# Optimization experiments

Hardware: AMD Instinct MI355X
Metric: run time of the kernel (lower is better)

Reference implementation:

```python
import jax, jax.numpy as jnp
import numpy as np

N = 16384   # total nodes in batch
E = 65536   # edges
B = 512     # sessions
L = 32      # nodes per session
H = 64      # hidden_size
HEADS = 16  # GAT heads (layer 1)
K = 3       # interests
V = 32000   # n_node (item vocab)
NEG = 0.2   # leaky relu slope


def _u(k, shape, stdv):
    return jax.random.uniform(k, shape, jnp.float32, -stdv, stdv)


def setup_inputs():
    key = jax.random.key(0)
    ks = jax.random.split(key, 24)
    s = 1.0 / np.sqrt(H)  # reset_parameters: uniform(-stdv, stdv)
    D = K * H
    return {
        "x": jax.random.randint(ks[0], (N,), 0, V),
        "edge_index": jax.random.randint(ks[1], (2, E), 0, N),
        "batch": jnp.repeat(jnp.arange(B, dtype=jnp.int32), L),
        "embedding": _u(ks[2], (V, H), s),
        "w_interest": _u(ks[3], (H, K), s),
        "gat1_W": _u(ks[4], (K, H, HEADS * H), s),
        "gat1_as": _u(ks[5], (K, HEADS, H), s),
        "gat1_ad": _u(ks[6], (K, HEADS, H), s),
        "gat1_b": _u(ks[7], (K, HEADS * H), s),
        "gat2_W": _u(ks[8], (K, HEADS * H, H), s),
        "gat2_as": _u(ks[9], (K, 1, H), s),
        "gat2_ad": _u(ks[10], (K, 1, H), s),
        "gat2_b": _u(ks[11], (K, H), s),
        "W1_w": _u(ks[12], (D, D), s), "W1_b": _u(ks[13], (D,), s),
        "W2_w": _u(ks[14], (D, D), s), "W2_b": _u(ks[15], (D,), s),
        "q_w": _u(ks[16], (D, 1), s), "q_b": _u(ks[17], (1,), s),
        "W3_w": _u(ks[18], (2 * D, D), s), "W3_b": _u(ks[19], (D,), s),
    }


def _gat(h_in, W, b, a_s, a_d, src, dst, valid, heads, out):
    """PyG GATConv: per-head linear, edge softmax over dest, self-loops for all nodes."""
    n = h_in.shape[0]
    h = (h_in @ W).reshape(n, heads, out)          # [n, heads, out]
    asrc = (h * a_s[None]).sum(-1)                 # [n, heads]
    adst = (h * a_d[None]).sum(-1)
    loop = jnp.arange(n)
    fs = jnp.concatenate([src, loop])              # edges + self-loops
    fd = jnp.concatenate([dst, loop])
    v = jnp.concatenate([valid, jnp.ones((n,), bool)])
    logits = jax.nn.leaky_relu(asrc[fs] + adst[fd], NEG)   # [E+n, heads]
    logits = jnp.where(v[:, None], logits, -1e9)
    m = jax.ops.segment_max(logits, fd, num_segments=n)
    p = jnp.exp(logits - m[fd]) * v[:, None]
    denom = jax.ops.segment_sum(p, fd, num_segments=n)     # [n, heads]
    num = jax.ops.segment_sum(p[:, :, None] * h[fs], fd, num_segments=n)
    return (num / denom[:, :, None]).reshape(n, heads * out) + b


def _model(x, edge_index, batch, embedding, w_interest,
           gat1_W, gat1_as, gat1_ad, gat1_b,
           gat2_W, gat2_as, gat2_ad, gat2_b,
           W1_w, W1_b, W2_w, W2_b, q_w, q_b, W3_w, W3_b):
    e = embedding[x]                                # [N, H]
    g = jax.nn.softmax((e @ w_interest) / 0.1, axis=-1)   # [N, K]
    mask = g > (1.0 / K)                            # interest_mask
    src, dst = edge_index[0], edge_index[1]
    hiddens = []
    for i in range(K):                              # fixed small interest loop
        xi = g[:, i:i + 1] * e                      # einsum('ik,il->ikl')[:, i]
        valid = mask[src, i] & mask[dst, i]         # subgraph edge mask
        h1 = jax.nn.relu(_gat(xi, gat1_W[i], gat1_b[i], gat1_as[i], gat1_ad[i],
                              src, dst, valid, HEADS, H))
        h2 = _gat(h1, gat2_W[i], gat2_b[i], gat2_as[i], gat2_ad[i],
                  src, dst, valid, 1, H)
        hiddens.append(h2)
    sess = jnp.concatenate(hiddens, axis=1)         # [N, K*H]
    # Embedding2Score
    last_idx = jax.ops.segment_max(jnp.arange(N), batch, num_segments=B)
    v_n = sess[last_idx]                            # [B, K*H]  last node per session
    q1 = v_n[batch] @ W1_w + W1_b                   # v_n repeated per node
    q2 = sess @ W2_w + W2_b
    alpha = jax.nn.sigmoid(q1 + q2) @ q_w + q_b     # [N, 1]
    s_g = jax.ops.segment_sum(alpha * sess, batch, num_segments=B)
    s_h = jnp.concatenate([v_n, s_g], axis=1) @ W3_w + W3_b   # [B, K*H]
    s_h = s_h.reshape(B * K, H)                     # multi-interest split
    z = s_h @ embedding.T                           # [B*K, V]
    return z.reshape(B, K, V).max(axis=1)           # [B, V]


def reference(x, edge_index, batch, embedding, w_interest,
              gat1_W, gat1_as, gat1_ad, gat1_b,
              gat2_W, gat2_as, gat2_ad, gat2_b,
              W1_w, W1_b, W2_w, W2_b, q_w, q_b, W3_w, W3_b):
    return _model(x, edge_index, batch, embedding, w_interest,
                  gat1_W, gat1_as, gat1_ad, gat1_b,
                  gat2_W, gat2_as, gat2_ad, gat2_b,
                  W1_w, W1_b, W2_w, W2_b, q_w, q_b, W3_w, W3_b)
```

## Files before the change

kernel.cpp:

```cpp
#include <hip/hip_runtime.h>
#include <math.h>

#define NN 16384
#define EE 65536
#define BB 512
#define VV 32000

typedef unsigned short us_t;
typedef unsigned int u32_t;
typedef __attribute__((ext_vector_type(4))) float f32x4;
typedef __attribute__((ext_vector_type(8))) short bf16x8;

__device__ __forceinline__ float bf2f(unsigned int u) {
  return __uint_as_float((u & 0xffffu) << 16);
}
__device__ __forceinline__ unsigned short f2bf(float f) {
  unsigned int x = __float_as_uint(f);
  unsigned int r = (x + 0x7fffu + ((x >> 16) & 1u)) >> 16;
  return (unsigned short)r;
}
__device__ __forceinline__ float wsum(float v) {
#pragma unroll
  for (int o = 32; o; o >>= 1) v += __shfl_xor(v, o, 64);
  return v;
}
__device__ __forceinline__ float redu16(float v) {
  v += __shfl_xor(v, 1, 64);
  v += __shfl_xor(v, 2, 64);
  v += __shfl_xor(v, 4, 64);
  v += __shfl_xor(v, 8, 64);
  return v;
}
__device__ __forceinline__ float lrelu(float x) { return x > 0.f ? x : 0.2f * x; }

__global__ void k_detect(const void* emb, int* flag) {
  if (threadIdx.x == 0 && blockIdx.x == 0) {
    const us_t* u = (const us_t*)emb;
    int ok = 1;
    for (int i = 0; i < 128; i++) {
      float v = bf2f((unsigned int)u[i]);
      if (!(fabsf(v) <= 0.13f)) { ok = 0; break; }
    }
    *flag = ok;
  }
}

struct PrepArgs {
  const void* src[17];
  void* dst[17];
  int n[17];
  int kind[17];
  int start[18];
};

__global__ void k_prep(PrepArgs pa, const int* __restrict__ flag) {
  int blk = blockIdx.x;
  int s = 0;
  while (s < 16 && blk >= pa.start[s + 1]) s++;
  int i = (blk - pa.start[s]) * 256 + threadIdx.x;
  if (i >= pa.n[s]) return;
  float v = (*flag) ? bf2f((unsigned int)((const us_t*)pa.src[s])[i])
                    : ((const float*)pa.src[s])[i];
  int kind = pa.kind[s];
  if (kind == 0) {
    ((float*)pa.dst[s])[i] = v;
  } else if (kind == 1) {
    ((us_t*)pa.dst[s])[i] = f2bf(v);
  } else if (kind == 2) {
    int ii = i >> 16, r = i & 65535, k = r >> 10, col = r & 1023;
    ((us_t*)pa.dst[s])[(ii << 16) + col * 64 + k] = f2bf(v);
  } else if (kind == 3) {
    int ii = i >> 16, r = i & 65535, k = r >> 6, col = r & 63;
    ((us_t*)pa.dst[s])[(ii << 16) + col * 1024 + k] = f2bf(v);
  } else {
    int k = i / 192, col = i % 192;
    ((us_t*)pa.dst[s])[col * 192 + k] = f2bf(v);
  }
}

__global__ void k_prepWa(const void* __restrict__ g1Wraw,
                         const float* __restrict__ g1as, const float* __restrict__ g1ad,
                         const int* __restrict__ flag, us_t* __restrict__ Waspack) {
  int gid = blockIdx.x * 256 + threadIdx.x;
  if (gid >= 96 * 64) return;
  int c = gid >> 6, k = gid & 63;
  int i = c >> 5, sd = (c >> 4) & 1, h = c & 15;
  const float* av = (sd ? g1ad : g1as) + i * 1024 + h * 64;
  size_t base = (size_t)i * 65536 + (size_t)k * 1024 + h * 64;
  int isbf = *flag;
  float s = 0.f;
  for (int d = 0; d < 64; d++) {
    float wv = isbf ? bf2f((unsigned int)((const us_t*)g1Wraw)[base + d])
                    : ((const float*)g1Wraw)[base + d];
    s += wv * av[d];
  }
  Waspack[c * 64 + k] = f2bf(s);
}

__global__ void k_embed(const int* __restrict__ x, const void* __restrict__ embr,
                        const void* __restrict__ wintr, const int* __restrict__ flag,
                        us_t* __restrict__ e_bf, float* __restrict__ g) {
  int gid = blockIdx.x * blockDim.x + threadIdx.x;
  int n = gid >> 6, lane = gid & 63;
  if (n >= NN) return;
  int isbf = *flag;
  size_t ei = (size_t)x[n] * 64 + lane;
  float v = isbf ? bf2f((unsigned int)((const us_t*)embr)[ei]) : ((const float*)embr)[ei];
  e_bf[(size_t)n * 64 + lane] = f2bf(v);
  float w0, w1, w2;
  if (isbf) {
    const us_t* w = (const us_t*)wintr;
    w0 = bf2f(w[lane * 3 + 0]); w1 = bf2f(w[lane * 3 + 1]); w2 = bf2f(w[lane * 3 + 2]);
  } else {
    const float* w = (const float*)wintr;
    w0 = w[lane * 3 + 0]; w1 = w[lane * 3 + 1]; w2 = w[lane * 3 + 2];
  }
  float t0 = wsum(v * w0), t1 = wsum(v * w1), t2 = wsum(v * w2);
  if (lane == 0) {
    float l0 = t0 / 0.1f, l1 = t1 / 0.1f, l2 = t2 / 0.1f;
    float m = fmaxf(l0, fmaxf(l1, l2));
    float p0 = __expf(l0 - m), p1 = __expf(l1 - m), p2 = __expf(l2 - m);
    float inv = 1.0f / (p0 + p1 + p2);
    g[n * 4 + 0] = p0 * inv; g[n * 4 + 1] = p1 * inv;
    g[n * 4 + 2] = p2 * inv; g[n * 4 + 3] = 0.f;
  }
}

__global__ void k_countv(const int* __restrict__ ei, const float* __restrict__ g,
                         int* __restrict__ countsv) {
  int e = blockIdx.x * 256 + threadIdx.x;
  if (e >= EE) return;
  int s = ei[e], d = ei[EE + e];
  const float thr = 1.0f / 3.0f;
#pragma unroll
  for (int i = 0; i < 3; i++) {
    if (g[s * 4 + i] > thr && g[d * 4 + i] > thr)
      atomicAdd(&countsv[i * NN + d], 1);
  }
}

__global__ void k_scanv(const int* __restrict__ counts, int* __restrict__ offsets) {
  __shared__ int part[256];
  __shared__ int excl[257];
  int t = threadIdx.x;
  int base = t * 192;
  int s = 0;
  for (int j = 0; j < 192; j++) s += counts[base + j];
  part[t] = s;
  __syncthreads();
  if (t == 0) {
    int run = 0;
    for (int j = 0; j < 256; j++) { excl[j] = run; run += part[j]; }
    excl[256] = run;
  }
  __syncthreads();
  int run = excl[t];
  for (int j = 0; j < 192; j++) { offsets[base + j] = run; run += counts[base + j]; }
  if (t == 255) offsets[3 * NN] = excl[256];
}

__global__ void k_fillv(const int* __restrict__ ei, const float* __restrict__ g,
                        const float* __restrict__ eatt,
                        const int* __restrict__ offsetsv, int* __restrict__ fillposv,
                        int2* __restrict__ edgesC, float* __restrict__ easrcP) {
  int e = blockIdx.x * 256 + threadIdx.x;
  if (e >= EE) return;
  int s = ei[e], d = ei[EE + e];
  const float thr = 1.0f / 3.0f;
#pragma unroll
  for (int i = 0; i < 3; i++) {
    float gs = g[s * 4 + i];
    if (gs > thr && g[d * 4 + i] > thr) {
      int pos = offsetsv[i * NN + d] + atomicAdd(&fillposv[i * NN + d], 1);
      edgesC[pos] = make_int2(s, __float_as_int(gs));
      const float* er = &eatt[(size_t)s * 96 + i * 32];
      float* op = &easrcP[(size_t)pos * 16];
#pragma unroll
      for (int h = 0; h < 16; h++) op[h] = gs * er[h];
    }
  }
}

__global__ __launch_bounds__(256) void k_easrc(
    const us_t* __restrict__ e_bf, const us_t* __restrict__ Waspack,
    float* __restrict__ eatt) {
  __shared__ char As[8192];
  int t = threadIdx.x;
  int row0 = blockIdx.x * 64;
  for (int id = t; id < 512; id += 256) {
    int r = id >> 3, c = id & 7;
    uint4 v = *(const uint4*)&e_bf[(size_t)(row0 + r) * 64 + c * 8];
    *(uint4*)(As + r * 128 + ((c ^ (r & 7)) << 4)) = v;
  }
  __syncthreads();
  int wv = t >> 6, L = t & 63, li = L & 15, lq = L >> 4;
#pragma unroll
  for (int ct = 0; ct < 6; ct++) {
    f32x4 acc = {0.f, 0.f, 0.f, 0.f};
#pragma unroll
    for (int ks = 0; ks < 2; ks++) {
      int row = wv * 16 + li;
      bf16x8 af = *(const bf16x8*)(As + row * 128 + (((ks * 4 + lq) ^ (row & 7)) << 4));
      bf16x8 bfr = *(const bf16x8*)(Waspack + (size_t)(ct * 16 + li) * 64 + ks * 32 + lq * 8);
      acc = __builtin_amdgcn_mfma_f32_16x16x32_bf16(af, bfr, acc, 0, 0, 0);
    }
#pragma unroll
    for (int r = 0; r < 4; r++) {
      int row = row0 + wv * 16 + lq * 4 + r;
      eatt[(size_t)row * 96 + ct * 16 + li] = acc[r];
    }
  }
}

__global__ __launch_bounds__(256) void k_gat_fused(
    const us_t* __restrict__ e_bf, const float* __restrict__ g,
    const float* __restrict__ eatt, const us_t* __restrict__ g1Wt,
    const us_t* __restrict__ g2Wt, const float* __restrict__ b1all,
    const float* __restrict__ g2as, const float* __restrict__ g2ad,
    const int* __restrict__ offsetsv, const int2* __restrict__ edgesC,
    const float* __restrict__ easrcP,
    float* __restrict__ h2pre, float* __restrict__ a2s, float* __restrict__ a2d) {
  __shared__ char xagg[32 * 2048];
  __shared__ char Tbuf[2][32 * 128];
  __shared__ float a2sl[32], a2dl[32];
  int t = threadIdx.x;
  int intr = blockIdx.y;
  int n0 = blockIdx.x * 32;
  int wv = t >> 6, L = t & 63, li = L & 15, lq = L >> 4;
  const us_t* Wt1 = g1Wt + (size_t)intr * 65536;
  const us_t* Wt2 = g2Wt + (size_t)intr * 65536;
  const float* b1 = b1all + intr * 1024;
  const float* as2 = g2as + intr * 64;
  const float* ad2 = g2ad + intr * 64;
  if (t < 32) { a2sl[t] = 0.f; a2dl[t] = 0.f; }
  int h = L >> 2;
  int doff = (L & 3) * 16;
  for (int k = 0; k < 8; k++) {
    int nl = wv * 8 + k;
    int n = n0 + nl;
    float gn = g[n * 4 + intr];
    float ad = gn * eatt[(size_t)n * 96 + intr * 32 + 16 + h];
    float m = lrelu(gn * eatt[(size_t)n * 96 + intr * 32 + h] + ad);
    float den = 1.f;
    float acc[16];
    {
      const uint4* ep = (const uint4*)&e_bf[(size_t)n * 64 + doff];
      uint4 a = ep[0], b = ep[1];
      acc[0] = gn * bf2f(a.x);  acc[1] = gn * bf2f(a.x >> 16);
      acc[2] = gn * bf2f(a.y);  acc[3] = gn * bf2f(a.y >> 16);
      acc[4] = gn * bf2f(a.z);  acc[5] = gn * bf2f(a.z >> 16);
      acc[6] = gn * bf2f(a.w);  acc[7] = gn * bf2f(a.w >> 16);
      acc[8] = gn * bf2f(b.x);  acc[9] = gn * bf2f(b.x >> 16);
      acc[10] = gn * bf2f(b.y); acc[11] = gn * bf2f(b.y >> 16);
      acc[12] = gn * bf2f(b.z); acc[13] = gn * bf2f(b.z >> 16);
      acc[14] = gn * bf2f(b.w); acc[15] = gn * bf2f(b.w >> 16);
    }
    int beg = offsetsv[intr * NN + n], end = offsetsv[intr * NN + n + 1];
    for (int j = beg; j < end; j++) {
      int2 sg = edgesC[j];
      int s = sg.x;
      float gs = __int_as_float(sg.y);
      float l = lrelu(easrcP[(size_t)j * 16 + h] + ad);
      float p = __expf(l - m);
      den += p;
      float pg = p * gs;
      const uint4* ep = (const uint4*)&e_bf[(size_t)s * 64 + doff];
      uint4 a = ep[0], b = ep[1];
      acc[0] += pg * bf2f(a.x);  acc[1] += pg * bf2f(a.x >> 16);
      acc[2] += pg * bf2f(a.y);  acc[3] += pg * bf2f(a.y >> 16);
      acc[4] += pg * bf2f(a.z);  acc[5] += pg * bf2f(a.z >> 16);
      acc[6] += pg * bf2f(a.w);  acc[7] += pg * bf2f(a.w >> 16);
      acc[8] += pg * bf2f(b.x);  acc[9] += pg * bf2f(b.x >> 16);
      acc[10] += pg * bf2f(b.y); acc[11] += pg * bf2f(b.y >> 16);
      acc[12] += pg * bf2f(b.z); acc[13] += pg * bf2f(b.z >> 16);
      acc[14] += pg * bf2f(b.w); acc[15] += pg * bf2f(b.w >> 16);
    }
    float inv = 1.f / den;
    u32_t w[8];
#pragma unroll
    for (int kk = 0; kk < 8; kk++) {
      w[kk] = (u32_t)f2bf(acc[2 * kk] * inv) | ((u32_t)f2bf(acc[2 * kk + 1] * inv) << 16);
    }
    int c0 = h * 8 + (L & 3) * 2;
    *(uint4*)(xagg + nl * 2048 + ((c0 ^ (nl & 7)) << 4)) = make_uint4(w[0], w[1], w[2], w[3]);
    *(uint4*)(xagg + nl * 2048 + (((c0 + 1) ^ (nl & 7)) << 4)) = make_uint4(w[4], w[5], w[6], w[7]);
  }
  __syncthreads();
  int rt = wv & 1, ctb = (wv >> 1) * 2;
  f32x4 acc2[2];
  acc2[0] = {0.f, 0.f, 0.f, 0.f};
  acc2[1] = {0.f, 0.f, 0.f, 0.f};
  for (int hh = 0; hh < 16; hh++) {
    f32x4 c1[2];
    c1[0] = {0.f, 0.f, 0.f, 0.f};
    c1[1] = {0.f, 0.f, 0.f, 0.f};
#pragma unroll
    for (int ks = 0; ks < 2; ks++) {
      int row = rt * 16 + li;
      int ca = hh * 8 + ks * 4 + lq;
      bf16x8 af = *(const bf16x8*)(xagg + row * 2048 + ((ca ^ (row & 7)) << 4));
#pragma unroll
      for (int c2 = 0; c2 < 2; c2++) {
        int oc = hh * 64 + (ctb + c2) * 16 + li;
        bf16x8 bfr = *(const bf16x8*)(Wt1 + (size_t)oc * 64 + ks * 32 + lq * 8);
        c1[c2] = __builtin_amdgcn_mfma_f32_16x16x32_bf16(af, bfr, c1[c2], 0, 0, 0);
      }
    }
    char* Tb = Tbuf[hh & 1];
#pragma unroll
    for (int c2 = 0; c2 < 2; c2++) {
      int col = (ctb + c2) * 16 + li;
      float bv = b1[hh * 64 + col];
#pragma unroll
      for (int r = 0; r < 4; r++) {
        int row = rt * 16 + lq * 4 + r;
        float tv = fmaxf(c1[c2][r] + bv, 0.f);
        int cc = (col * 2) >> 4;
        *(us_t*)(Tb + row * 128 + ((cc ^ (row & 7)) << 4) + ((col * 2) & 15)) = f2bf(tv);
      }
    }
    __syncthreads();
#pragma unroll
    for (int ks = 0; ks < 2; ks++) {
      int row = rt * 16 + li;
      int cc = ks * 4 + lq;
      bf16x8 af2 = *(const bf16x8*)(Tb + row * 128 + ((cc ^ (row & 7)) << 4));
#pragma unroll
      for (int c2 = 0; c2 < 2; c2++) {
        int oc = (ctb + c2) * 16 + li;
        bf16x8 bfr = *(const bf16x8*)(Wt2 + (size_t)oc * 1024 + hh * 64 + ks * 32 + lq * 8);
        acc2[c2] = __builtin_amdgcn_mfma_f32_16x16x32_bf16(af2, bfr, acc2[c2], 0, 0, 0);
      }
    }
  }
  float ps[4] = {0.f, 0.f, 0.f, 0.f}, pd[4] = {0.f, 0.f, 0.f, 0.f};
#pragma unroll
  for (int c2 = 0; c2 < 2; c2++) {
    int col = (ctb + c2) * 16 + li;
    float asv = as2[col], adv = ad2[col];
#pragma unroll
    for (int r = 0; r < 4; r++) {
      int row = rt * 16 + lq * 4 + r;
      float v = acc2[c2][r];
      h2pre[((size_t)intr * NN + n0 + row) * 64 + col] = v;
      ps[r] += v * asv;
      pd[r] += v * adv;
    }
  }
#pragma unroll
  for (int r = 0; r < 4; r++) { ps[r] = redu16(ps[r]); pd[r] = redu16(pd[r]); }
  if (li == 0) {
#pragma unroll
    for (int r = 0; r < 4; r++) {
      atomicAdd(&a2sl[rt * 16 + lq * 4 + r], ps[r]);
      atomicAdd(&a2dl[rt * 16 + lq * 4 + r], pd[r]);
    }
  }
  __syncthreads();
  if (t < 32) {
    a2s[(size_t)intr * NN + n0 + t] = a2sl[t];
    a2d[(size_t)intr * NN + n0 + t] = a2dl[t];
  }
}

__global__ void k_gat2_agg(const float* __restrict__ h2pre_a,
                           const float* __restrict__ a2s_a, const float* __restrict__ a2d_a,
                           const float* __restrict__ b2all,
                           const int* __restrict__ offsetsv,
                           const int2* __restrict__ edgesC, float* __restrict__ sess) {
  int intr = blockIdx.y;
  int gid = blockIdx.x * blockDim.x + threadIdx.x;
  int n = gid >> 6, lane = gid & 63;
  if (n >= NN) return;
  const float* h2pre = h2pre_a + (size_t)intr * NN * 64;
  const float* a2s = a2s_a + (size_t)intr * NN;
  const float* a2d = a2d_a + (size_t)intr * NN;
  const float* b2 = b2all + intr * 64;
  float ad = a2d[n];
  float m = lrelu(a2s[n] + ad);
  float den = 1.f;
  float acc = h2pre[(size_t)n * 64 + lane];
  int beg = offsetsv[intr * NN + n], end = offsetsv[intr * NN + n + 1];
  for (int j = beg; j < end; j++) {
    int s = edgesC[j].x;
    float l = lrelu(a2s[s] + ad);
    float p = __expf(l - m);
    den += p;
    acc += p * h2pre[(size_t)s * 64 + lane];
  }
  sess[(size_t)n * 192 + intr * 64 + lane] = acc / den + b2[lane];
}

__global__ __launch_bounds__(192) void k_vq1(
    const float* __restrict__ sess,
    const float* __restrict__ W1w, const float* __restrict__ W1b,
    float* __restrict__ vn, float* __restrict__ vq1) {
  __shared__ float row[192];
  int b = blockIdx.x, j = threadIdx.x;
  int li = b * 32 + 31;
  float v = sess[(size_t)li * 192 + j];
  row[j] = v;
  vn[b * 192 + j] = v;
  __syncthreads();
  float acc = W1b[j];
  for (int k = 0; k < 192; k++) acc += row[k] * W1w[k * 192 + j];
  vq1[b * 192 + j] = acc;
}

__global__ __launch_bounds__(256) void k_alpha_sg_mfma(
    const float* __restrict__ sess, const float* __restrict__ vq1,
    const us_t* __restrict__ W2T, const float* __restrict__ W2b,
    const float* __restrict__ qw, const float* __restrict__ qb,
    float* __restrict__ sg) {
  __shared__ char As[64 * 512];
  __shared__ float vq_l[2 * 192];
  __shared__ float w2b_l[192], qw_l[192];
  __shared__ float sg_l[2 * 192];
  int t = threadIdx.x;
  int n0 = blockIdx.x * 64;
  if (t < 192) { w2b_l[t] = W2b[t]; qw_l[t] = qw[t]; }
  for (int id = t; id < 384; id += 256) {
    sg_l[id] = 0.f;
    vq_l[id] = vq1[(size_t)(blockIdx.x * 2) * 192 + id];
  }
  for (int id = t; id < 1536; id += 256) {
    int r = id / 24, c = id % 24;
    const float* p = &sess[(size_t)(n0 + r) * 192 + c * 8];
    float4 f0 = *(const float4*)p;
    float4 f1 = *(const float4*)(p + 4);
    u32_t w0 = (u32_t)f2bf(f0.x) | ((u32_t)f2bf(f0.y) << 16);
    u32_t w1 = (u32_t)f2bf(f0.z) | ((u32_t)f2bf(f0.w) << 16);
    u32_t w2 = (u32_t)f2bf(f1.x) | ((u32_t)f2bf(f1.y) << 16);
    u32_t w3 = (u32_t)f2bf(f1.z) | ((u32_t)f2bf(f1.w) << 16);
    *(uint4*)(As + r * 512 + ((c ^ (r & 7)) << 4)) = make_uint4(w0, w1, w2, w3);
  }
  __syncthreads();
  int wv = t >> 6, lane = t & 63, li = lane & 15, lq = lane >> 4;
  int sl = wv >> 1;
  f32x4 acc[12];
#pragma unroll
  for (int sub = 0; sub < 12; sub++) acc[sub] = {0.f, 0.f, 0.f, 0.f};
#pragma unroll
  for (int ks = 0; ks < 6; ks++) {
    int r = wv * 16 + li;
    bf16x8 af = *(const bf16x8*)(As + r * 512 + (((ks * 4 + lq) ^ (r & 7)) << 4));
#pragma unroll
    for (int sub = 0; sub < 12; sub++) {
      bf16x8 bfr = *(const bf16x8*)&W2T[(size_t)(sub * 16 + li) * 192 + ks * 32 + lq * 8];
      acc[sub] = __builtin_amdgcn_mfma_f32_16x16x32_bf16(af, bfr, acc[sub], 0, 0, 0);
    }
  }
  float qbv = qb[0];
  float s_part[12];
#pragma unroll
  for (int sub = 0; sub < 12; sub++) s_part[sub] = 0.f;
#pragma unroll
  for (int rr = 0; rr < 4; rr++) {
    int n = n0 + wv * 16 + lq * 4 + rr;
    float ap = 0.f;
    float sv[12];
#pragma unroll
    for (int sub = 0; sub < 12; sub++) {
      int col = sub * 16 + li;
      float q = vq_l[sl * 192 + col] + acc[sub][rr] + w2b_l[col];
      float sgm = 1.f / (1.f + __expf(-q));
      ap += sgm * qw_l[col];
      sv[sub] = sess[(size_t)n * 192 + col];
    }
    ap = redu16(ap);
    float alpha = ap + qbv;
#pragma unroll
    for (int sub = 0; sub < 12; sub++) s_part[sub] += alpha * sv[sub];
  }
#pragma unroll
  for (int sub = 0; sub < 12; sub++) {
    float v = s_part[sub];
    v += __shfl_xor(v, 16, 64);
    v += __shfl_xor(v, 32, 64);
    if (lq == 0) atomicAdd(&sg_l[sl * 192 + sub * 16 + li], v);
  }
  __syncthreads();
  for (int id = t; id < 384; id += 256)
    sg[(size_t)(blockIdx.x * 2) * 192 + id] = sg_l[id];
}

__global__ __launch_bounds__(192) void k_sh(
    const float* __restrict__ vn, const float* __restrict__ sg,
    const float* __restrict__ W3w, const float* __restrict__ W3b,
    float* __restrict__ sh) {
  __shared__ float row[384];
  int b = blockIdx.x, j = threadIdx.x;
  row[j] = vn[b * 192 + j];
  row[192 + j] = sg[b * 192 + j];
  __syncthreads();
  float acc = W3b[j];
  for (int k = 0; k < 384; k++) acc += row[k] * W3w[k * 192 + j];
  sh[b * 192 + j] = acc;
}

__global__ __launch_bounds__(256) void k_final_mfma(
    const float* __restrict__ sh, const us_t* __restrict__ emb_bf,
    void* __restrict__ out, const int* __restrict__ flag) {
  __shared__ uint4 AsU[384];
  __shared__ uint4 BsU[2048];
  char* As = (char*)AsU;
  char* Bs = (char*)BsU;
  int t = threadIdx.x;
  int v0 = blockIdx.x * 256, b0 = blockIdx.y * 16;
  for (int id = t; id < 384; id += 256) {
    int i2 = id >> 7, rem = id & 127, r = rem >> 3, c = rem & 7;
    const float* p = &sh[(size_t)(b0 + r) * 192 + i2 * 64 + c * 8];
    float4 f0 = *(const float4*)p;
    float4 f1 = *(const float4*)(p + 4);
    u32_t w0 = (u32_t)f2bf(f0.x) | ((u32_t)f2bf(f0.y) << 16);
    u32_t w1 = (u32_t)f2bf(f0.z) | ((u32_t)f2bf(f0.w) << 16);
    u32_t w2 = (u32_t)f2bf(f1.x) | ((u32_t)f2bf(f1.y) << 16);
    u32_t w3 = (u32_t)f2bf(f1.z) | ((u32_t)f2bf(f1.w) << 16);
    *(uint4*)(As + i2 * 2048 + r * 128 + ((c ^ (r & 7)) << 4)) = make_uint4(w0, w1, w2, w3);
  }
  for (int id = t; id < 2048; id += 256) {
    int vr = id >> 3, c = id & 7;
    uint4 v = *(const uint4*)&emb_bf[(size_t)(v0 + vr) * 64 + c * 8];
    *(uint4*)(Bs + vr * 128 + ((c ^ (vr & 7)) << 4)) = v;
  }
  __syncthreads();
  int wv = t >> 6, lane = t & 63, li = lane & 15, lq = lane >> 4;
  int cb = wv * 64;
  int isbf = *flag;
  f32x4 acc[3][4];
#pragma unroll
  for (int i = 0; i < 3; i++)
#pragma unroll
    for (int sub = 0; sub < 4; sub++) acc[i][sub] = {0.f, 0.f, 0.f, 0.f};
#pragma unroll
  for (int ks = 0; ks < 2; ks++) {
    bf16x8 bfr[4];
#pragma unroll
    for (int sub = 0; sub < 4; sub++) {
      int vr = cb + sub * 16 + li;
      bfr[sub] = *(const bf16x8*)(Bs + vr * 128 + ((((ks << 2) | lq) ^ (vr & 7)) << 4));
    }
#pragma unroll
    for (int i = 0; i < 3; i++) {
      bf16x8 af = *(const bf16x8*)(As + i * 2048 + li * 128 + ((((ks << 2) | lq) ^ (li & 7)) << 4));
#pragma unroll
      for (int sub = 0; sub < 4; sub++)
        acc[i][sub] = __builtin_amdgcn_mfma_f32_16x16x32_bf16(af, bfr[sub], acc[i][sub], 0, 0, 0);
    }
  }
#pragma unroll
  for (int sub = 0; sub < 4; sub++) {
    int col = v0 + cb + sub * 16 + li;
#pragma unroll
    for (int rr = 0; rr < 4; rr++) {
      float o = fmaxf(fmaxf(acc[0][sub][rr], acc[1][sub][rr]), acc[2][sub][rr]);
      int b = b0 + lq * 4 + rr;
      if (isbf) ((us_t*)out)[(size_t)b * VV + col] = f2bf(o);
      else ((float*)out)[(size_t)b * VV + col] = o;
    }
  }
}

extern "C" void kernel_launch(void* const* d_in, const int* in_sizes, int n_in,
                              void* d_out, int out_size, void* d_ws, size_t ws_size,
                              hipStream_t stream) {
  if (n_in < 21) return;
  const int* x = (const int*)d_in[0];
  const int* ei = (const int*)d_in[1];

  char* ws = (char*)d_ws;
  size_t off = 0;
  auto A = [&](size_t bytes) -> char* {
    char* p = ws + off;
    off += (bytes + 255) & ~(size_t)255;
    return p;
  };
  int* flag = (int*)A(4);
  us_t* emb_bf = (us_t*)A((size_t)VV * 64 * 2);
  us_t* e_bf = (us_t*)A((size_t)NN * 64 * 2);
  us_t* g1Wt = (us_t*)A((size_t)3 * 65536 * 2);
  us_t* g2Wt = (us_t*)A((size_t)3 * 65536 * 2);
  us_t* W2T = (us_t*)A((size_t)36864 * 2);
  us_t* Waspack = (us_t*)A((size_t)96 * 64 * 2);
  float* eatt = (float*)A((size_t)NN * 96 * 4);
  float* c_g1as = (float*)A(3072 * 4);
  float* c_g1ad = (float*)A(3072 * 4);
  float* c_g1b = (float*)A(3072 * 4);
  float* c_g2as = (float*)A(192 * 4);
  float* c_g2ad = (float*)A(192 * 4);
  float* c_g2b = (float*)A(192 * 4);
  float* c_W1w = (float*)A(36864 * 4);
  float* c_W1b = (float*)A(192 * 4);
  float* c_W2b = (float*)A(192 * 4);
  float* c_qw = (float*)A(192 * 4);
  float* c_qb = (float*)A(4);
  float* c_W3w = (float*)A(73728 * 4);
  float* c_W3b = (float*)A(192 * 4);
  float* g_buf = (float*)A((size_t)NN * 4 * 4);
  float* h2pre = (float*)A((size_t)3 * NN * 64 * 4);
  float* a2s = (float*)A((size_t)3 * NN * 4);
  float* a2d = (float*)A((size_t)3 * NN * 4);
  float* sess = (float*)A((size_t)NN * 192 * 4);
  float* vq1 = (float*)A((size_t)BB * 192 * 4);
  float* sg = (float*)A((size_t)BB * 192 * 4);
  float* vn = (float*)A((size_t)BB * 192 * 4);
  float* shb = (float*)A((size_t)BB * 192 * 4);
  int* countsv = (int*)A((size_t)3 * NN * 4);
  int* offsetsv = (int*)A((size_t)(3 * NN + 1) * 4);
  int* fillposv = (int*)A((size_t)3 * NN * 4);
  int2* edgesC = (int2*)A((size_t)3 * EE * 8);
  float* easrcP = (float*)A((size_t)3 * EE * 16 * 4);
  if (off > ws_size) return;

  hipMemsetAsync(countsv, 0, 3 * NN * 4, stream);
  hipMemsetAsync(fillposv, 0, 3 * NN * 4, stream);

  k_detect<<<1, 64, 0, stream>>>(d_in[3], flag);

  PrepArgs pa;
  int nb = 0, idx = 0;
  auto SEC = [&](const void* s, void* d, int n, int kind) {
    pa.src[idx] = s; pa.dst[idx] = d; pa.n[idx] = n; pa.kind[idx] = kind;
    pa.start[idx] = nb; nb += (n + 255) / 256; idx++;
  };
  SEC(d_in[3], emb_bf, VV * 64, 1);
  SEC(d_in[5], g1Wt, 196608, 2);
  SEC(d_in[9], g2Wt, 196608, 3);
  SEC(d_in[15], W2T, 36864, 4);
  SEC(d_in[6], c_g1as, 3072, 0);
  SEC(d_in[7], c_g1ad, 3072, 0);
  SEC(d_in[8], c_g1b, 3072, 0);
  SEC(d_in[10], c_g2as, 192, 0);
  SEC(d_in[11], c_g2ad, 192, 0);
  SEC(d_in[12], c_g2b, 192, 0);
  SEC(d_in[13], c_W1w, 36864, 0);
  SEC(d_in[14], c_W1b, 192, 0);
  SEC(d_in[16], c_W2b, 192, 0);
  SEC(d_in[17], c_qw, 192, 0);
  SEC(d_in[18], c_qb, 1, 0);
  SEC(d_in[19], c_W3w, 73728, 0);
  SEC(d_in[20], c_W3b, 192, 0);
  pa.start[17] = nb;
  k_prep<<<nb, 256, 0, stream>>>(pa, flag);
  k_prepWa<<<24, 256, 0, stream>>>(d_in[5], c_g1as, c_g1ad, flag, Waspack);

  k_embed<<<NN * 64 / 256, 256, 0, stream>>>(x, d_in[3], d_in[4], flag, e_bf, g_buf);
  k_easrc<<<NN / 64, 256, 0, stream>>>(e_bf, Waspack, eatt);
  k_countv<<<EE / 256, 256, 0, stream>>>(ei, g_buf, countsv);
  k_scanv<<<1, 256, 0, stream>>>(countsv, offsetsv);
  k_fillv<<<EE / 256, 256, 0, stream>>>(ei, g_buf, eatt, offsetsv, fillposv,
                                        edgesC, easrcP);

  k_gat_fused<<<dim3(NN / 32, 3), 256, 0, stream>>>(
      e_bf, g_buf, eatt, g1Wt, g2Wt, c_g1b, c_g2as, c_g2ad,
      offsetsv, edgesC, easrcP, h2pre, a2s, a2d);
  k_gat2_agg<<<dim3(NN * 64 / 256, 3), 256, 0, stream>>>(
      h2pre, a2s, a2d, c_g2b, offsetsv, edgesC, sess);

  k_vq1<<<BB, 192, 0, stream>>>(sess, c_W1w, c_W1b, vn, vq1);
  k_alpha_sg_mfma<<<NN / 64, 256, 0, stream>>>(sess, vq1, W2T, c_W2b, c_qw, c_qb, sg);
  k_sh<<<BB, 192, 0, stream>>>(vn, sg, c_W3w, c_W3b, shb);
  k_final_mfma<<<dim3(VV / 256, BB / 16), 256, 0, stream>>>(shb, emb_bf, d_out, flag);
}
```

Measured before the change: 301.9 us.

## Split GAT fused MLP across heads per wave with 16-node blocks

The fused GAT kernel now processes 16 nodes per block instead of 32, doubling the grid. Each wave owns four of the 16 heads and computes all 64 output columns for them, using per-wave transpose buffers. This removes the block-wide barrier inside the head loop, replacing it with a local LDS waitcnt. Partial layer-2 outputs are reduced across waves with shared-memory float atomics, then the attention dot products are computed per row with wave reductions. The cost is more atomics and more redundant weight loads per node.

New measurement: 339.0 us. 1.12x slower.

```diff
diff --git a/kernel.cpp b/kernel.cpp
--- a/kernel.cpp
+++ b/kernel.cpp
@@ -220,23 +220,23 @@
     const int* __restrict__ offsetsv, const int2* __restrict__ edgesC,
     const float* __restrict__ easrcP,
     float* __restrict__ h2pre, float* __restrict__ a2s, float* __restrict__ a2d) {
-  __shared__ char xagg[32 * 2048];
-  __shared__ char Tbuf[2][32 * 128];
-  __shared__ float a2sl[32], a2dl[32];
+  __shared__ char xagg[16 * 2048];
+  __shared__ char Tbuf[4][2][16 * 128];
+  __shared__ float h2red[16 * 64];
   int t = threadIdx.x;
   int intr = blockIdx.y;
-  int n0 = blockIdx.x * 32;
+  int n0 = blockIdx.x * 16;
   int wv = t >> 6, L = t & 63, li = L & 15, lq = L >> 4;
   const us_t* Wt1 = g1Wt + (size_t)intr * 65536;
   const us_t* Wt2 = g2Wt + (size_t)intr * 65536;
   const float* b1 = b1all + intr * 1024;
   const float* as2 = g2as + intr * 64;
   const float* ad2 = g2ad + intr * 64;
-  if (t < 32) { a2sl[t] = 0.f; a2dl[t] = 0.f; }
+  for (int id = t; id < 1024; id += 256) h2red[id] = 0.f;
   int h = L >> 2;
   int doff = (L & 3) * 16;
-  for (int k = 0; k < 8; k++) {
-    int nl = wv * 8 + k;
+  for (int k = 0; k < 4; k++) {
+    int nl = wv * 4 + k;
     int n = n0 + nl;
     float gn = g[n * 4 + intr];
     float ad = gn * eatt[(size_t)n * 96 + intr * 32 + 16 + h];
@@ -286,80 +286,73 @@
     *(uint4*)(xagg + nl * 2048 + (((c0 + 1) ^ (nl & 7)) << 4)) = make_uint4(w[4], w[5], w[6], w[7]);
   }
   __syncthreads();
-  int rt = wv & 1, ctb = (wv >> 1) * 2;
-  f32x4 acc2[2];
-  acc2[0] = {0.f, 0.f, 0.f, 0.f};
-  acc2[1] = {0.f, 0.f, 0.f, 0.f};
-  for (int hh = 0; hh < 16; hh++) {
-    f32x4 c1[2];
-    c1[0] = {0.f, 0.f, 0.f, 0.f};
-    c1[1] = {0.f, 0.f, 0.f, 0.f};
+  f32x4 acc2[4];
+#pragma unroll
+  for (int ct = 0; ct < 4; ct++) acc2[ct] = {0.f, 0.f, 0.f, 0.f};
+  for (int hi = 0; hi < 4; hi++) {
+    int hh = wv * 4 + hi;
+    f32x4 c1[4];
+#pragma unroll
+    for (int ct = 0; ct < 4; ct++) c1[ct] = {0.f, 0.f, 0.f, 0.f};
 #pragma unroll
     for (int ks = 0; ks < 2; ks++) {
-      int row = rt * 16 + li;
       int ca = hh * 8 + ks * 4 + lq;
-      bf16x8 af = *(const bf16x8*)(xagg + row * 2048 + ((ca ^ (row & 7)) << 4));
-#pragma unroll
-      for (int c2 = 0; c2 < 2; c2++) {
-        int oc = hh * 64 + (ctb + c2) * 16 + li;
+      bf16x8 af = *(const bf16x8*)(xagg + li * 2048 + ((ca ^ (li & 7)) << 4));
+#pragma unroll
+      for (int ct = 0; ct < 4; ct++) {
+        int oc = hh * 64 + ct * 16 + li;
         bf16x8 bfr = *(const bf16x8*)(Wt1 + (size_t)oc * 64 + ks * 32 + lq * 8);
-        c1[c2] = __builtin_amdgcn_mfma_f32_16x16x32_bf16(af, bfr, c1[c2], 0, 0, 0);
+        c1[ct] = __builtin_amdgcn_mfma_f32_16x16x32_bf16(af, bfr, c1[ct], 0, 0, 0);
       }
     }
-    char* Tb = Tbuf[hh & 1];
-#pragma unroll
-    for (int c2 = 0; c2 < 2; c2++) {
-      int col = (ctb + c2) * 16 + li;
+    char* Tb = Tbuf[wv][hi & 1];
+#pragma unroll
+    for (int ct = 0; ct < 4; ct++) {
+      int col = ct * 16 + li;
       float bv = b1[hh * 64 + col];
 #pragma unroll
       for (int r = 0; r < 4; r++) {
-        int row = rt * 16 + lq * 4 + r;
-        float tv = fmaxf(c1[c2][r] + bv, 0.f);
-        int cc = (col * 2) >> 4;
-        *(us_t*)(Tb + row * 128 + ((cc ^ (row & 7)) << 4) + ((col * 2) & 15)) = f2bf(tv);
+        int row = lq * 4 + r;
+        float tv = fmaxf(c1[ct][r] + bv, 0.f);
+        int byte = col * 2;
+        *(us_t*)(Tb + row * 128 + (((byte >> 4) ^ (row & 7)) << 4) + (byte & 15)) = f2bf(tv);
       }
     }
-    __syncthreads();
+    asm volatile("s_waitcnt lgkmcnt(0)" ::: "memory");
+    __builtin_amdgcn_sched_barrier(0);
 #pragma unroll
     for (int ks = 0; ks < 2; ks++) {
-      int row = rt * 16 + li;
       int cc = ks * 4 + lq;
-      bf16x8 af2 = *(const bf16x8*)(Tb + row * 128 + ((cc ^ (row & 7)) << 4));
-#pragma unroll
-      for (int c2 = 0; c2 < 2; c2++) {
-        int oc = (ctb + c2) * 16 + li;
+      bf16x8 af2 = *(const bf16x8*)(Tb + li * 128 + ((cc ^ (li & 7)) << 4));
+#pragma unroll
+      for (int ct = 0; ct < 4; ct++) {
+        int oc = ct * 16 + li;
         bf16x8 bfr = *(const bf16x8*)(Wt2 + (size_t)oc * 1024 + hh * 64 + ks * 32 + lq * 8);
-        acc2[c2] = __builtin_amdgcn_mfma_f32_16x16x32_bf16(af2, bfr, acc2[c2], 0, 0, 0);
+        acc2[ct] = __builtin_amdgcn_mfma_f32_16x16x32_bf16(af2, bfr, acc2[ct], 0, 0, 0);
       }
     }
   }
-  float ps[4] = {0.f, 0.f, 0.f, 0.f}, pd[4] = {0.f, 0.f, 0.f, 0.f};
-#pragma unroll
-  for (int c2 = 0; c2 < 2; c2++) {
-    int col = (ctb + c2) * 16 + li;
-    float asv = as2[col], adv = ad2[col];
+#pragma unroll
+  for (int ct = 0; ct < 4; ct++) {
+    int col = ct * 16 + li;
 #pragma unroll
     for (int r = 0; r < 4; r++) {
-      int row = rt * 16 + lq * 4 + r;
-      float v = acc2[c2][r];
-      h2pre[((size_t)intr * NN + n0 + row) * 64 + col] = v;
-      ps[r] += v * asv;
-      pd[r] += v * adv;
-    }
-  }
-#pragma unroll
-  for (int r = 0; r < 4; r++) { ps[r] = redu16(ps[r]); pd[r] = redu16(pd[r]); }
-  if (li == 0) {
-#pragma unroll
-    for (int r = 0; r < 4; r++) {
-      atomicAdd(&a2sl[rt * 16 + lq * 4 + r], ps[r]);
-      atomicAdd(&a2dl[rt * 16 + lq * 4 + r], pd[r]);
-    }
-  }
-  __syncthreads();
-  if (t < 32) {
-    a2s[(size_t)intr * NN + n0 + t] = a2sl[t];
-    a2d[(size_t)intr * NN + n0 + t] = a2dl[t];
+      int row = lq * 4 + r;
+      atomicAdd(&h2red[row * 64 + col], acc2[ct][r]);
+    }
+  }
+  __syncthreads();
+#pragma unroll
+  for (int rr = 0; rr < 4; rr++) {
+    int row = wv * 4 + rr;
+    float val = h2red[row * 64 + L];
+    h2pre[((size_t)intr * NN + n0 + row) * 64 + L] = val;
+    float ps = wsum(val * as2[L]);
+    float pd = wsum(val * ad2[L]);
+    if (L == 0) {
+      a2s[(size_t)intr * NN + n0 + row] = ps;
+      a2d[(size_t)intr * NN + n0 + row] = pd;
+    }
   }
 }
 
@@ -651,7 +644,7 @@
   k_fillv<<<EE / 256, 256, 0, stream>>>(ei, g_buf, eatt, offsetsv, fillposv,
                                         edgesC, easrcP);
 
-  k_gat_fused<<<dim3(NN / 32, 3), 256, 0, stream>>>(
+  k_gat_fused<<<dim3(NN / 16, 3), 256, 0, stream>>>(
       e_bf, g_buf, eatt, g1Wt, g2Wt, c_g1b, c_g2as, c_g2ad,
       offsetsv, edgesC, easrcP, h2pre, a2s, a2d);
   k_gat2_agg<<<dim3(NN * 64 / 256, 3), 256, 0, stream>>>(
```
